# Kernel optimization log

Measured on AMD Instinct MI355X. Metric: run time of the kernel, lower is better.

## Reference

```python
import jax, jax.numpy as jnp
import numpy as np

L, B, E, H = 2048, 4, 1024, 8
D1 = 2 * E  # expand_ratio * embed_dim, already divisible by H
EPS = 1e-8


def setup_inputs() -> dict:
    key = jax.random.key(0)
    ks = jax.random.split(key, 12)
    std = 0.02
    return {
        "query": jax.random.normal(ks[0], (L, B, E), jnp.float32),
        "key": jax.random.normal(ks[1], (L, B, E), jnp.float32),
        "value": jax.random.normal(ks[2], (L, B, E), jnp.float32),
        "u_w": jax.random.normal(ks[3], (D1, E), jnp.float32) * std,
        "u_b": jax.random.normal(ks[4], (D1,), jnp.float32) * std,
        "v_w": jax.random.normal(ks[5], (D1, E), jnp.float32) * std,
        "v_b": jax.random.normal(ks[6], (D1,), jnp.float32) * std,
        "o_w": jax.random.normal(ks[7], (E, D1), jnp.float32) * std,
        "o_b": jax.random.normal(ks[8], (E,), jnp.float32) * std,
        # Toeplitz relative-position coefficients: t_0 (zero), t_1..t_{n-1} (pos), t_{-1}..t_{-(n-1)} (neg)
        "pos": jax.random.normal(ks[9], (H, L - 1), jnp.float32) * std,
        "zero": jax.random.normal(ks[10], (H, 1), jnp.float32) * std,
        "neg": jax.random.normal(ks[11], (H, L - 1), jnp.float32) * std,
    }


def _toeplitz_mix(v, pos, zero, neg):
    # v: (b, h, n, d). y_i = sum_j t_{i-j} v_j via circular conv of length 2n.
    b, h, n, d = v.shape
    m = 2 * n
    # a[0]=t_0, a[1:n]=t_1..t_{n-1}, a[n]=0 (unused), a[n+1:2n]=t_{-(n-1)}..t_{-1}
    a = jnp.concatenate([zero, pos[:, : n - 1], jnp.zeros((h, 1), v.dtype), neg[:, : n - 1][:, ::-1]], axis=-1)
    af = jnp.fft.rfft(a, n=m, axis=-1)            # (h, n+1)
    vf = jnp.fft.rfft(v, n=m, axis=-2)            # (b, h, n+1, d)
    y = jnp.fft.irfft(af[None, :, :, None] * vf, n=m, axis=-2)
    return y[:, :, :n, :]


def reference(query, key, value, u_w, u_b, v_w, v_b, o_w, o_b, pos, zero, neg):
    n, b, e = query.shape
    # SimpleRMSNorm: x / (||x||_2 / sqrt(d) + eps)
    rms = jnp.linalg.norm(query, axis=-1, keepdims=True) * (e ** -0.5)
    x = query / (rms + EPS)
    u = jax.nn.silu(jnp.einsum("nbe,fe->nbf", x, u_w) + u_b)   # (n, b, d1)
    v = jax.nn.silu(jnp.einsum("nbe,fe->nbf", x, v_w) + v_b)   # (n, b, d1)
    hd = v.shape[-1] // H
    vh = v.reshape(n, b, H, hd).transpose(1, 2, 0, 3)          # (b, h, n, d)
    y = _toeplitz_mix(vh, pos, zero, neg)                      # (b, h, n, d)
    y = y.transpose(2, 0, 1, 3).reshape(n, b, H * hd)          # (n, b, d1)
    out = u * y
    return jnp.einsum("nbf,ef->nbe", out, o_w) + o_b + query
```

## Files before the change

kernel.cpp:

```cpp
#include <hip/hip_runtime.h>
#include <math.h>

typedef unsigned short u16;
typedef __bf16 bf16x8 __attribute__((ext_vector_type(8)));
typedef float f32x4 __attribute__((ext_vector_type(4)));

#define LSEQ 2048
#define NB   4
#define NE   1024
#define NHEAD 8
#define ND1  2048
#define NHD  256
#define NM   8192
#define CRP  4104

__device__ __forceinline__ u16 f2bf(float f) {
  unsigned u = __float_as_uint(f);
  u += 0x7FFFu + ((u >> 16) & 1u);
  return (u16)(u >> 16);
}
__device__ __forceinline__ float bf2f(u16 h) {
  return __uint_as_float(((unsigned)h) << 16);
}

__device__ __forceinline__ void gl_lds16(const u16* g, u16* l) {
  __builtin_amdgcn_global_load_lds(
      (const __attribute__((address_space(1))) void*)g,
      (__attribute__((address_space(3))) void*)l, 16, 0, 0);
}

__global__ __launch_bounds__(256) void cvt_kernel(const float* __restrict__ src,
                                                  u16* __restrict__ dst, int n4) {
  int i = blockIdx.x * 256 + threadIdx.x;
  if (i < n4) {
    float4 v = ((const float4*)src)[i];
    ushort4 o;
    o.x = f2bf(v.x); o.y = f2bf(v.y); o.z = f2bf(v.z); o.w = f2bf(v.w);
    ((ushort4*)dst)[i] = o;
  }
}

__global__ __launch_bounds__(256) void build_cr8(const float* __restrict__ pos,
                                                 const float* __restrict__ zero,
                                                 const float* __restrict__ neg,
                                                 u16* __restrict__ cr8) {
  int h = blockIdx.x >> 3, s = blockIdx.x & 7;
  u16* out = cr8 + (size_t)blockIdx.x * CRP;
  for (int m = threadIdx.x; m < CRP; m += 256) {
    int mm = m + s;
    float val = 0.f;
    if (mm <= 4094) {
      int t = 2047 - mm;
      if (t == 0)      val = zero[h];
      else if (t > 0)  val = pos[h * (LSEQ - 1) + t - 1];
      else             val = neg[h * (LSEQ - 1) + (-t) - 1];
    }
    out[m] = f2bf(val);
  }
}

__global__ __launch_bounds__(256) void rmsnorm_kernel(const float* __restrict__ q,
                                                      u16* __restrict__ x) {
  int row = blockIdx.x;
  float4 v = ((const float4*)(q + (size_t)row * NE))[threadIdx.x];
  float ss = v.x * v.x + v.y * v.y + v.z * v.z + v.w * v.w;
  #pragma unroll
  for (int off = 32; off > 0; off >>= 1) ss += __shfl_down(ss, off, 64);
  __shared__ float wss[4];
  int wave = threadIdx.x >> 6, lane = threadIdx.x & 63;
  if (lane == 0) wss[wave] = ss;
  __syncthreads();
  float tot = wss[0] + wss[1] + wss[2] + wss[3];
  float scale = 1.f / (sqrtf(tot) * 0.03125f + 1e-8f);
  ushort4 o;
  o.x = f2bf(v.x * scale); o.y = f2bf(v.y * scale);
  o.z = f2bf(v.z * scale); o.w = f2bf(v.w * scale);
  ((ushort4*)(x + (size_t)row * NE))[threadIdx.x] = o;
}

__global__ __launch_bounds__(256) void transpose_v(const u16* __restrict__ v,
                                                   u16* __restrict__ vT) {
  __shared__ u16 s[64 * 66];
  int j0 = blockIdx.x * 64, d0 = blockIdx.y * 64;
  int h = blockIdx.z >> 2, b = blockIdx.z & 3;
  #pragma unroll
  for (int it = 0; it < 16; ++it) {
    int idx = threadIdx.x + 256 * it;
    int r = idx >> 6, c = idx & 63;
    s[r * 66 + c] = v[((size_t)(j0 + r) * NB + b) * ND1 + h * NHD + d0 + c];
  }
  __syncthreads();
  #pragma unroll
  for (int it = 0; it < 16; ++it) {
    int idx = threadIdx.x + 256 * it;
    int r = idx >> 6, c = idx & 63;
    vT[((size_t)h * (NB * NHD) + b * NHD + d0 + r) * LSEQ + j0 + c] = s[c * 66 + r];
  }
}


__device__ __forceinline__ bf16x8 ldsfrag(const u16* buf, int rr, int q) {
  return *(const bf16x8*)(buf + rr * 64 + ((q ^ (rr & 7)) * 8));
}

template <int MODE>
__device__ __forceinline__ void stage_Ah(const u16* A, const u16* Acr, int Ksz,
                                         int i0, int kt, int half, u16* dstbuf,
                                         int tid) {
  int wave = tid >> 6;
  #pragma unroll
  for (int it = 0; it < 2; ++it) {
    int vv = it * 512 + tid;
    int r = vv >> 3, c8 = vv & 7, c8s = c8 ^ (r & 7);
    int row = i0 + half * 128 + r;
    const u16* src;
    if (MODE != 1) {
      src = A + (size_t)row * Ksz + kt * 64 + c8s * 8;
    } else {
      int p = 2047 - row + kt * 64;
      int s = p & 7, qq = p - s;
      src = Acr + (size_t)s * CRP + qq + c8s * 8;
    }
    gl_lds16(src, dstbuf + half * 8192 + (it * 512 + wave * 64) * 8);
  }
}

__device__ __forceinline__ void stage_Bh(const u16* B, int Ksz, int n0, int kt,
                                         int half, u16* dstbuf, int tid) {
  int wave = tid >> 6;
  #pragma unroll
  for (int it = 0; it < 2; ++it) {
    int vv = it * 512 + tid;
    int r = vv >> 3, c8 = vv & 7, c8s = c8 ^ (r & 7);
    gl_lds16(B + (size_t)(n0 + half * 128 + r) * Ksz + kt * 64 + c8s * 8,
             dstbuf + half * 8192 + (it * 512 + wave * 64) * 8);
  }
}

#define PHASE_MID()                                        \
  __builtin_amdgcn_s_barrier();                            \
  asm volatile("s_waitcnt lgkmcnt(0)" ::: "memory");       \
  __builtin_amdgcn_sched_barrier(0);                       \
  __builtin_amdgcn_s_setprio(1);

#define PHASE_END()                                        \
  __builtin_amdgcn_s_setprio(0);                           \
  __builtin_amdgcn_s_barrier();                            \
  __builtin_amdgcn_sched_barrier(0);

template <int MODE>
__global__ __launch_bounds__(512, 2) void gemm256(
    const u16* __restrict__ A, const u16* __restrict__ Bw,
    const float* __restrict__ bias, u16* __restrict__ Cbf,
    int Msz, int Nsz, int Ksz) {
  extern __shared__ __align__(16) u16 lds[];
  u16* As = lds;
  u16* Ws = lds + 32768;

  const int tid = threadIdx.x;
  const int lane = tid & 63, wave = tid >> 6;
  const int wr = (wave >> 2) * 128, wc = (wave & 3) * 64;
  const int lr = lane & 15, lq = lane >> 4;
  const int i0 = blockIdx.y * 256, n0 = blockIdx.x * 256;

  const u16* Bh = Bw;
  const u16* Acr = A;
  if (MODE == 1) {
    Bh  = Bw + (size_t)blockIdx.z * Nsz * Ksz;
    Acr = A + (size_t)blockIdx.z * 8 * CRP;
  }
  const int nkt = Ksz >> 6;

  f32x4 acc[8][4];
  #pragma unroll
  for (int a = 0; a < 8; ++a)
    #pragma unroll
    for (int b = 0; b < 4; ++b) acc[a][b] = (f32x4){0.f, 0.f, 0.f, 0.f};

  stage_Ah<MODE>(A, Acr, Ksz, i0, 0, 0, As, tid);
  stage_Ah<MODE>(A, Acr, Ksz, i0, 0, 1, As, tid);
  stage_Bh(Bh, Ksz, n0, 0, 0, Ws, tid);
  stage_Bh(Bh, Ksz, n0, 0, 1, Ws, tid);
  stage_Bh(Bh, Ksz, n0, 1, 0, Ws + 16384, tid);
  stage_Bh(Bh, Ksz, n0, 1, 1, Ws + 16384, tid);
  asm volatile("s_waitcnt vmcnt(4)" ::: "memory");
  __builtin_amdgcn_s_barrier();
  __builtin_amdgcn_sched_barrier(0);

  for (int tt = 0; tt < nkt; ++tt) {
    const int cur = tt & 1;
    const u16* Ab = As + cur * 16384;
    const u16* Wb = Ws + cur * 16384;
    u16* An = As + (cur ^ 1) * 16384;
    u16* Wn = Ws + cur * 16384;

    bf16x8 a[4][2], b[2][2], b2[2][2];

    #pragma unroll
    for (int rt = 0; rt < 4; ++rt) {
      int ar = wr + rt * 16 + lr;
      a[rt][0] = ldsfrag(Ab, ar, lq);
      a[rt][1] = ldsfrag(Ab, ar, 4 + lq);
    }
    #pragma unroll
    for (int ct = 0; ct < 2; ++ct) {
      int br = wc + ct * 16 + lr;
      b[ct][0] = ldsfrag(Wb, br, lq);
      b[ct][1] = ldsfrag(Wb, br, 4 + lq);
    }
    if (tt + 1 < nkt) stage_Ah<MODE>(A, Acr, Ksz, i0, tt + 1, 0, An, tid);
    PHASE_MID();
    #pragma unroll
    for (int rt = 0; rt < 4; ++rt)
      #pragma unroll
      for (int ct = 0; ct < 2; ++ct) {
        acc[rt][ct] = __builtin_amdgcn_mfma_f32_16x16x32_bf16(a[rt][0], b[ct][0], acc[rt][ct], 0, 0, 0);
        acc[rt][ct] = __builtin_amdgcn_mfma_f32_16x16x32_bf16(a[rt][1], b[ct][1], acc[rt][ct], 0, 0, 0);
      }
    PHASE_END();

    #pragma unroll
    for (int ct = 0; ct < 2; ++ct) {
      int br = wc + (ct + 2) * 16 + lr;
      b2[ct][0] = ldsfrag(Wb, br, lq);
      b2[ct][1] = ldsfrag(Wb, br, 4 + lq);
    }
    if (tt + 1 < nkt) stage_Ah<MODE>(A, Acr, Ksz, i0, tt + 1, 1, An, tid);
    PHASE_MID();
    #pragma unroll
    for (int rt = 0; rt < 4; ++rt)
      #pragma unroll
      for (int ct = 0; ct < 2; ++ct) {
        acc[rt][ct + 2] = __builtin_amdgcn_mfma_f32_16x16x32_bf16(a[rt][0], b2[ct][0], acc[rt][ct + 2], 0, 0, 0);
        acc[rt][ct + 2] = __builtin_amdgcn_mfma_f32_16x16x32_bf16(a[rt][1], b2[ct][1], acc[rt][ct + 2], 0, 0, 0);
      }
    PHASE_END();

    #pragma unroll
    for (int rt = 0; rt < 4; ++rt) {
      int ar = wr + (rt + 4) * 16 + lr;
      a[rt][0] = ldsfrag(Ab, ar, lq);
      a[rt][1] = ldsfrag(Ab, ar, 4 + lq);
    }
    if (tt + 2 < nkt) stage_Bh(Bh, Ksz, n0, tt + 2, 0, Wn, tid);
    PHASE_MID();
    #pragma unroll
    for (int rt = 0; rt < 4; ++rt)
      #pragma unroll
      for (int ct = 0; ct < 2; ++ct) {
        acc[rt + 4][ct + 2] = __builtin_amdgcn_mfma_f32_16x16x32_bf16(a[rt][0], b2[ct][0], acc[rt + 4][ct + 2], 0, 0, 0);
        acc[rt + 4][ct + 2] = __builtin_amdgcn_mfma_f32_16x16x32_bf16(a[rt][1], b2[ct][1], acc[rt + 4][ct + 2], 0, 0, 0);
      }
    PHASE_END();

    if (tt + 2 < nkt) stage_Bh(Bh, Ksz, n0, tt + 2, 1, Wn, tid);
    if (tt == nkt - 2) { asm volatile("s_waitcnt vmcnt(0)" ::: "memory"); }
    else               { asm volatile("s_waitcnt vmcnt(4)" ::: "memory"); }
    PHASE_MID();
    #pragma unroll
    for (int rt = 0; rt < 4; ++rt)
      #pragma unroll
      for (int ct = 0; ct < 2; ++ct) {
        acc[rt + 4][ct] = __builtin_amdgcn_mfma_f32_16x16x32_bf16(a[rt][0], b[ct][0], acc[rt + 4][ct], 0, 0, 0);
        acc[rt + 4][ct] = __builtin_amdgcn_mfma_f32_16x16x32_bf16(a[rt][1], b[ct][1], acc[rt + 4][ct], 0, 0, 0);
      }
    PHASE_END();
  }

  #pragma unroll
  for (int rt = 0; rt < 8; ++rt) {
    #pragma unroll
    for (int ct = 0; ct < 4; ++ct) {
      int col = n0 + wc + ct * 16 + lr;
      #pragma unroll
      for (int reg = 0; reg < 4; ++reg) {
        int row = i0 + wr + rt * 16 + lq * 4 + reg;
        float yv = acc[rt][ct][reg];
        if (MODE == 0) {
          float t = yv + bias[col];
          t = t / (1.f + __expf(-t));
          Cbf[(size_t)row * Nsz + col] = f2bf(t);
        } else {
          int b = col >> 8, d = col & 255;
          size_t ui = ((size_t)row * NB + b) * ND1 + (size_t)blockIdx.z * NHD + d;
          float uv = bf2f(Cbf[ui]);
          Cbf[ui] = f2bf(uv * yv);
        }
      }
    }
  }
}

template <int MODE>
__global__ __launch_bounds__(256) void gemm_kernel(
    const u16* __restrict__ A, const u16* __restrict__ Bw,
    const float* __restrict__ bias, const float* __restrict__ resid,
    u16* __restrict__ Cbf, float* __restrict__ Cf,
    int Msz, int Nsz, int Ksz) {
  __shared__ __align__(16) u16 As[128 * 64];
  __shared__ __align__(16) u16 Ws[128 * 64];

  const int tid = threadIdx.x;
  const int lane = tid & 63, wave = tid >> 6;
  const int wr = (wave >> 1) * 64, wc = (wave & 1) * 64;
  const int lr = lane & 15, lq = lane >> 4;
  const int i0 = blockIdx.y * 128, n0 = blockIdx.x * 128;

  f32x4 acc[4][4];
  #pragma unroll
  for (int a = 0; a < 4; ++a)
    #pragma unroll
    for (int b = 0; b < 4; ++b) acc[a][b] = (f32x4){0.f, 0.f, 0.f, 0.f};

  const int nkt = Ksz >> 6;
  for (int kt = 0; kt < nkt; ++kt) {
    #pragma unroll
    for (int it = 0; it < 4; ++it) {
      int vv = tid + 256 * it;
      int r = vv >> 3, c8 = vv & 7;
      int c8s = c8 ^ (r & 7);
      gl_lds16(A + (size_t)(i0 + r) * Ksz + kt * 64 + c8s * 8,
               &As[(size_t)(wave * 64 + it * 256) * 8]);
    }
    #pragma unroll
    for (int it = 0; it < 4; ++it) {
      int vv = tid + 256 * it;
      int r = vv >> 3, c8 = vv & 7;
      int c8s = c8 ^ (r & 7);
      gl_lds16(Bw + (size_t)(n0 + r) * Ksz + kt * 64 + c8s * 8,
               &Ws[(size_t)(wave * 64 + it * 256) * 8]);
    }
    __syncthreads();
    #pragma unroll
    for (int ks = 0; ks < 2; ++ks) {
      bf16x8 af[4], bfr[4];
      #pragma unroll
      for (int rt = 0; rt < 4; ++rt) {
        int ar = wr + rt * 16 + lr;
        int cq = (ks * 4 + lq) ^ (ar & 7);
        af[rt] = *(const bf16x8*)&As[ar * 64 + cq * 8];
      }
      #pragma unroll
      for (int ct = 0; ct < 4; ++ct) {
        int br = wc + ct * 16 + lr;
        int cq = (ks * 4 + lq) ^ (br & 7);
        bfr[ct] = *(const bf16x8*)&Ws[br * 64 + cq * 8];
      }
      #pragma unroll
      for (int rt = 0; rt < 4; ++rt)
        #pragma unroll
        for (int ct = 0; ct < 4; ++ct)
          acc[rt][ct] = __builtin_amdgcn_mfma_f32_16x16x32_bf16(
              af[rt], bfr[ct], acc[rt][ct], 0, 0, 0);
    }
    __syncthreads();
  }

  #pragma unroll
  for (int rt = 0; rt < 4; ++rt) {
    #pragma unroll
    for (int ct = 0; ct < 4; ++ct) {
      int col = n0 + wc + ct * 16 + lr;
      #pragma unroll
      for (int reg = 0; reg < 4; ++reg) {
        int row = i0 + wr + rt * 16 + lq * 4 + reg;
        float yv = acc[rt][ct][reg];
        size_t oi = (size_t)row * Nsz + col;
        Cf[oi] = yv + bias[col] + resid[oi];
      }
    }
  }
}

extern "C" void kernel_launch(void* const* d_in, const int* in_sizes, int n_in,
                              void* d_out, int out_size, void* d_ws, size_t ws_size,
                              hipStream_t stream) {
  const float* q    = (const float*)d_in[0];
  const float* uw   = (const float*)d_in[3];
  const float* ub   = (const float*)d_in[4];
  const float* vw   = (const float*)d_in[5];
  const float* vb   = (const float*)d_in[6];
  const float* ow   = (const float*)d_in[7];
  const float* ob   = (const float*)d_in[8];
  const float* pos  = (const float*)d_in[9];
  const float* zero = (const float*)d_in[10];
  const float* neg  = (const float*)d_in[11];
  float* out = (float*)d_out;

  char* ws = (char*)d_ws;
  u16* x   = (u16*)(ws + 0);
  u16* uwb = (u16*)(ws + 16777216);
  u16* vwb = (u16*)(ws + 20971520);
  u16* owb = (u16*)(ws + 25165824);
  u16* u   = (u16*)(ws + 29360128);
  u16* v   = (u16*)(ws + 62914560);
  u16* vT  = (u16*)(ws + 96468992);
  u16* cr8 = (u16*)(ws + 130023424);

  hipFuncSetAttribute((const void*)gemm256<0>,
                      hipFuncAttributeMaxDynamicSharedMemorySize, 131072);
  hipFuncSetAttribute((const void*)gemm256<1>,
                      hipFuncAttributeMaxDynamicSharedMemorySize, 131072);

  cvt_kernel<<<2048, 256, 0, stream>>>(uw, uwb, 524288);
  cvt_kernel<<<2048, 256, 0, stream>>>(vw, vwb, 524288);
  cvt_kernel<<<2048, 256, 0, stream>>>(ow, owb, 524288);
  build_cr8<<<64, 256, 0, stream>>>(pos, zero, neg, cr8);
  rmsnorm_kernel<<<NM, 256, 0, stream>>>(q, x);

  gemm256<0><<<dim3(8, 32, 1), 512, 131072, stream>>>(x, uwb, ub, u, NM, ND1, NE);
  gemm256<0><<<dim3(8, 32, 1), 512, 131072, stream>>>(x, vwb, vb, v, NM, ND1, NE);
  transpose_v<<<dim3(32, 4, 32), 256, 0, stream>>>(v, vT);
  gemm256<1><<<dim3(4, 8, 8), 512, 131072, stream>>>(cr8, vT, nullptr, u,
                                                     LSEQ, NB * NHD, LSEQ);
  gemm_kernel<2><<<dim3(8, 64, 1), 256, 0, stream>>>(u, owb, ob, q, nullptr, out,
                                                     NM, NE, ND1);
}
```

Before: 373.2 us.

## Merge prep kernels, batch U/V GEMMs, restage epilogue through LDS, vectorize transpose

Merges the three weight conversions and the Toeplitz-coefficient build into one launch, and runs the U and V projections as a single grid with a z-dimension that picks the weight, bias and output. The 256-tile GEMM main loop drops from four phases to two per k-step, loading all B fragments at once. The epilogue goes through a swizzled LDS tile so global stores and the u*y multiply use 16-byte vector accesses. The transpose now uses ushort4 loads and stores. Together these aim to cut launch count and scattered 2-byte stores, at the cost of more registers and less interleaving of loads with MFMA work.

```diff
diff --git a/kernel.cpp b/kernel.cpp
--- a/kernel.cpp
+++ b/kernel.cpp
@@ -22,6 +22,11 @@
 __device__ __forceinline__ float bf2f(u16 h) {
   return __uint_as_float(((unsigned)h) << 16);
 }
+__device__ __forceinline__ unsigned mulbf2(unsigned y2, unsigned u2) {
+  float ylo = bf2f((u16)(y2 & 0xFFFF)), yhi = bf2f((u16)(y2 >> 16));
+  float ulo = bf2f((u16)(u2 & 0xFFFF)), uhi = bf2f((u16)(u2 >> 16));
+  return (unsigned)f2bf(ylo * ulo) | ((unsigned)f2bf(yhi * uhi) << 16);
+}
 
 __device__ __forceinline__ void gl_lds16(const u16* g, u16* l) {
   __builtin_amdgcn_global_load_lds(
@@ -29,33 +34,36 @@
       (__attribute__((address_space(3))) void*)l, 16, 0, 0);
 }
 
-__global__ __launch_bounds__(256) void cvt_kernel(const float* __restrict__ src,
-                                                  u16* __restrict__ dst, int n4) {
-  int i = blockIdx.x * 256 + threadIdx.x;
-  if (i < n4) {
-    float4 v = ((const float4*)src)[i];
+__global__ __launch_bounds__(256) void prep_kernel(
+    const float* __restrict__ uw, const float* __restrict__ vw,
+    const float* __restrict__ ow, u16* __restrict__ uwb, u16* __restrict__ vwb,
+    u16* __restrict__ owb, const float* __restrict__ pos,
+    const float* __restrict__ zero, const float* __restrict__ neg,
+    u16* __restrict__ cr8) {
+  int bx = blockIdx.x;
+  if (bx < 6144) {
+    const float* s = bx < 2048 ? uw : (bx < 4096 ? vw : ow);
+    u16* d = bx < 2048 ? uwb : (bx < 4096 ? vwb : owb);
+    int i = (bx & 2047) * 256 + threadIdx.x;
+    float4 v = ((const float4*)s)[i];
     ushort4 o;
     o.x = f2bf(v.x); o.y = f2bf(v.y); o.z = f2bf(v.z); o.w = f2bf(v.w);
-    ((ushort4*)dst)[i] = o;
-  }
-}
-
-__global__ __launch_bounds__(256) void build_cr8(const float* __restrict__ pos,
-                                                 const float* __restrict__ zero,
-                                                 const float* __restrict__ neg,
-                                                 u16* __restrict__ cr8) {
-  int h = blockIdx.x >> 3, s = blockIdx.x & 7;
-  u16* out = cr8 + (size_t)blockIdx.x * CRP;
-  for (int m = threadIdx.x; m < CRP; m += 256) {
-    int mm = m + s;
-    float val = 0.f;
-    if (mm <= 4094) {
-      int t = 2047 - mm;
-      if (t == 0)      val = zero[h];
-      else if (t > 0)  val = pos[h * (LSEQ - 1) + t - 1];
-      else             val = neg[h * (LSEQ - 1) + (-t) - 1];
-    }
-    out[m] = f2bf(val);
+    ((ushort4*)d)[i] = o;
+  } else {
+    int bb = bx - 6144;
+    int h = bb >> 3, sh = bb & 7;
+    u16* out = cr8 + (size_t)bb * CRP;
+    for (int m = threadIdx.x; m < CRP; m += 256) {
+      int mm = m + sh;
+      float val = 0.f;
+      if (mm <= 4094) {
+        int t = 2047 - mm;
+        if (t == 0)      val = zero[h];
+        else if (t > 0)  val = pos[h * (LSEQ - 1) + t - 1];
+        else             val = neg[h * (LSEQ - 1) + (-t) - 1];
+      }
+      out[m] = f2bf(val);
+    }
   }
 }
 
@@ -80,21 +88,27 @@
 
 __global__ __launch_bounds__(256) void transpose_v(const u16* __restrict__ v,
                                                    u16* __restrict__ vT) {
-  __shared__ u16 s[64 * 66];
+  __shared__ u16 s[64 * 68];
   int j0 = blockIdx.x * 64, d0 = blockIdx.y * 64;
   int h = blockIdx.z >> 2, b = blockIdx.z & 3;
   #pragma unroll
-  for (int it = 0; it < 16; ++it) {
-    int idx = threadIdx.x + 256 * it;
-    int r = idx >> 6, c = idx & 63;
-    s[r * 66 + c] = v[((size_t)(j0 + r) * NB + b) * ND1 + h * NHD + d0 + c];
+  for (int it = 0; it < 4; ++it) {
+    int idx = it * 256 + threadIdx.x;
+    int r = idx >> 4, c4 = idx & 15;
+    *(ushort4*)&s[r * 68 + c4 * 4] =
+        *(const ushort4*)&v[((size_t)(j0 + r) * NB + b) * ND1 + h * NHD + d0 + c4 * 4];
   }
   __syncthreads();
   #pragma unroll
-  for (int it = 0; it < 16; ++it) {
-    int idx = threadIdx.x + 256 * it;
-    int r = idx >> 6, c = idx & 63;
-    vT[((size_t)h * (NB * NHD) + b * NHD + d0 + r) * LSEQ + j0 + c] = s[c * 66 + r];
+  for (int it = 0; it < 4; ++it) {
+    int idx = it * 256 + threadIdx.x;
+    int cc = idx >> 4, jq = idx & 15;
+    ushort4 o;
+    o.x = s[(jq * 4 + 0) * 68 + cc];
+    o.y = s[(jq * 4 + 1) * 68 + cc];
+    o.z = s[(jq * 4 + 2) * 68 + cc];
+    o.w = s[(jq * 4 + 3) * 68 + cc];
+    *(ushort4*)&vT[((size_t)h * (NB * NHD) + b * NHD + d0 + cc) * LSEQ + j0 + jq * 4] = o;
   }
 }
 
@@ -150,9 +164,10 @@
 
 template <int MODE>
 __global__ __launch_bounds__(512, 2) void gemm256(
-    const u16* __restrict__ A, const u16* __restrict__ Bw,
-    const float* __restrict__ bias, u16* __restrict__ Cbf,
-    int Msz, int Nsz, int Ksz) {
+    const u16* __restrict__ A, const u16* __restrict__ Bw0,
+    const u16* __restrict__ Bw1, const float* __restrict__ bias0,
+    const float* __restrict__ bias1, u16* __restrict__ C0,
+    u16* __restrict__ C1, int Msz, int Nsz, int Ksz) {
   extern __shared__ __align__(16) u16 lds[];
   u16* As = lds;
   u16* Ws = lds + 32768;
@@ -163,10 +178,16 @@
   const int lr = lane & 15, lq = lane >> 4;
   const int i0 = blockIdx.y * 256, n0 = blockIdx.x * 256;
 
-  const u16* Bh = Bw;
+  const u16* Bh;
   const u16* Acr = A;
-  if (MODE == 1) {
-    Bh  = Bw + (size_t)blockIdx.z * Nsz * Ksz;
+  const float* bias = bias0;
+  u16* Cp = C0;
+  if (MODE == 0) {
+    Bh = blockIdx.z ? Bw1 : Bw0;
+    bias = blockIdx.z ? bias1 : bias0;
+    Cp = blockIdx.z ? C1 : C0;
+  } else {
+    Bh  = Bw0 + (size_t)blockIdx.z * Nsz * Ksz;
     Acr = A + (size_t)blockIdx.z * 8 * CRP;
   }
   const int nkt = Ksz >> 6;
@@ -194,7 +215,7 @@
     u16* An = As + (cur ^ 1) * 16384;
     u16* Wn = Ws + cur * 16384;
 
-    bf16x8 a[4][2], b[2][2], b2[2][2];
+    bf16x8 a[4][2], b[4][2];
 
     #pragma unroll
     for (int rt = 0; rt < 4; ++rt) {
@@ -203,36 +224,22 @@
       a[rt][1] = ldsfrag(Ab, ar, 4 + lq);
     }
     #pragma unroll
-    for (int ct = 0; ct < 2; ++ct) {
+    for (int ct = 0; ct < 4; ++ct) {
       int br = wc + ct * 16 + lr;
       b[ct][0] = ldsfrag(Wb, br, lq);
       b[ct][1] = ldsfrag(Wb, br, 4 + lq);
     }
-    if (tt + 1 < nkt) stage_Ah<MODE>(A, Acr, Ksz, i0, tt + 1, 0, An, tid);
+    if (tt + 1 < nkt) {
+      stage_Ah<MODE>(A, Acr, Ksz, i0, tt + 1, 0, An, tid);
+      stage_Ah<MODE>(A, Acr, Ksz, i0, tt + 1, 1, An, tid);
+    }
     PHASE_MID();
     #pragma unroll
     for (int rt = 0; rt < 4; ++rt)
       #pragma unroll
-      for (int ct = 0; ct < 2; ++ct) {
+      for (int ct = 0; ct < 4; ++ct) {
         acc[rt][ct] = __builtin_amdgcn_mfma_f32_16x16x32_bf16(a[rt][0], b[ct][0], acc[rt][ct], 0, 0, 0);
         acc[rt][ct] = __builtin_amdgcn_mfma_f32_16x16x32_bf16(a[rt][1], b[ct][1], acc[rt][ct], 0, 0, 0);
-      }
-    PHASE_END();
-
-    #pragma unroll
-    for (int ct = 0; ct < 2; ++ct) {
-      int br = wc + (ct + 2) * 16 + lr;
-      b2[ct][0] = ldsfrag(Wb, br, lq);
-      b2[ct][1] = ldsfrag(Wb, br, 4 + lq);
-    }
-    if (tt + 1 < nkt) stage_Ah<MODE>(A, Acr, Ksz, i0, tt + 1, 1, An, tid);
-    PHASE_MID();
-    #pragma unroll
-    for (int rt = 0; rt < 4; ++rt)
-      #pragma unroll
-      for (int ct = 0; ct < 2; ++ct) {
-        acc[rt][ct + 2] = __builtin_amdgcn_mfma_f32_16x16x32_bf16(a[rt][0], b2[ct][0], acc[rt][ct + 2], 0, 0, 0);
-        acc[rt][ct + 2] = __builtin_amdgcn_mfma_f32_16x16x32_bf16(a[rt][1], b2[ct][1], acc[rt][ct + 2], 0, 0, 0);
       }
     PHASE_END();
 
@@ -242,61 +249,68 @@
       a[rt][0] = ldsfrag(Ab, ar, lq);
       a[rt][1] = ldsfrag(Ab, ar, 4 + lq);
     }
-    if (tt + 2 < nkt) stage_Bh(Bh, Ksz, n0, tt + 2, 0, Wn, tid);
-    PHASE_MID();
-    #pragma unroll
-    for (int rt = 0; rt < 4; ++rt)
-      #pragma unroll
-      for (int ct = 0; ct < 2; ++ct) {
-        acc[rt + 4][ct + 2] = __builtin_amdgcn_mfma_f32_16x16x32_bf16(a[rt][0], b2[ct][0], acc[rt + 4][ct + 2], 0, 0, 0);
-        acc[rt + 4][ct + 2] = __builtin_amdgcn_mfma_f32_16x16x32_bf16(a[rt][1], b2[ct][1], acc[rt + 4][ct + 2], 0, 0, 0);
-      }
-    PHASE_END();
-
-    if (tt + 2 < nkt) stage_Bh(Bh, Ksz, n0, tt + 2, 1, Wn, tid);
+    if (tt + 2 < nkt) {
+      stage_Bh(Bh, Ksz, n0, tt + 2, 0, Wn, tid);
+      stage_Bh(Bh, Ksz, n0, tt + 2, 1, Wn, tid);
+    }
     if (tt == nkt - 2) { asm volatile("s_waitcnt vmcnt(0)" ::: "memory"); }
     else               { asm volatile("s_waitcnt vmcnt(4)" ::: "memory"); }
     PHASE_MID();
     #pragma unroll
     for (int rt = 0; rt < 4; ++rt)
       #pragma unroll
-      for (int ct = 0; ct < 2; ++ct) {
+      for (int ct = 0; ct < 4; ++ct) {
         acc[rt + 4][ct] = __builtin_amdgcn_mfma_f32_16x16x32_bf16(a[rt][0], b[ct][0], acc[rt + 4][ct], 0, 0, 0);
         acc[rt + 4][ct] = __builtin_amdgcn_mfma_f32_16x16x32_bf16(a[rt][1], b[ct][1], acc[rt + 4][ct], 0, 0, 0);
       }
     PHASE_END();
   }
 
+  __syncthreads();
+  u16* zl = lds;
   #pragma unroll
   for (int rt = 0; rt < 8; ++rt) {
     #pragma unroll
     for (int ct = 0; ct < 4; ++ct) {
-      int col = n0 + wc + ct * 16 + lr;
+      int col_l = wc + ct * 16 + lr;
       #pragma unroll
       for (int reg = 0; reg < 4; ++reg) {
-        int row = i0 + wr + rt * 16 + lq * 4 + reg;
+        int row_l = wr + rt * 16 + lq * 4 + reg;
         float yv = acc[rt][ct][reg];
         if (MODE == 0) {
-          float t = yv + bias[col];
-          t = t / (1.f + __expf(-t));
-          Cbf[(size_t)row * Nsz + col] = f2bf(t);
-        } else {
-          int b = col >> 8, d = col & 255;
-          size_t ui = ((size_t)row * NB + b) * ND1 + (size_t)blockIdx.z * NHD + d;
-          float uv = bf2f(Cbf[ui]);
-          Cbf[ui] = f2bf(uv * yv);
+          float t = yv + bias[n0 + col_l];
+          yv = t / (1.f + __expf(-t));
         }
-      }
-    }
-  }
-}
-
-template <int MODE>
-__global__ __launch_bounds__(256) void gemm_kernel(
+        zl[row_l * 256 + (col_l ^ (((row_l >> 2) & 3) << 4))] = f2bf(yv);
+      }
+    }
+  }
+  __syncthreads();
+  #pragma unroll
+  for (int k = 0; k < 16; ++k) {
+    int cc = k * 512 + tid;
+    int row_l = cc >> 5, c8 = cc & 31;
+    int colbase = c8 * 8;
+    int swz = colbase ^ (((row_l >> 2) & 3) << 4);
+    uint4 y4 = *(uint4*)&zl[row_l * 256 + swz];
+    if (MODE == 0) {
+      *(uint4*)&Cp[(size_t)(i0 + row_l) * Nsz + n0 + colbase] = y4;
+    } else {
+      size_t ui = ((size_t)(i0 + row_l) * NB + blockIdx.x) * ND1 +
+                  (size_t)blockIdx.z * NHD + colbase;
+      uint4 u4 = *(const uint4*)&Cp[ui];
+      uint4 o;
+      o.x = mulbf2(y4.x, u4.x); o.y = mulbf2(y4.y, u4.y);
+      o.z = mulbf2(y4.z, u4.z); o.w = mulbf2(y4.w, u4.w);
+      *(uint4*)&Cp[ui] = o;
+    }
+  }
+}
+
+__global__ __launch_bounds__(256) void gemm_out(
     const u16* __restrict__ A, const u16* __restrict__ Bw,
     const float* __restrict__ bias, const float* __restrict__ resid,
-    u16* __restrict__ Cbf, float* __restrict__ Cf,
-    int Msz, int Nsz, int Ksz) {
+    float* __restrict__ Cf, int Nsz, int Ksz) {
   __shared__ __align__(16) u16 As[128 * 64];
   __shared__ __align__(16) u16 Ws[128 * 64];
 
@@ -364,9 +378,8 @@
       #pragma unroll
       for (int reg = 0; reg < 4; ++reg) {
         int row = i0 + wr + rt * 16 + lq * 4 + reg;
-        float yv = acc[rt][ct][reg];
         size_t oi = (size_t)row * Nsz + col;
-        Cf[oi] = yv + bias[col] + resid[oi];
+        Cf[oi] = acc[rt][ct][reg] + bias[col] + resid[oi];
       }
     }
   }
@@ -402,17 +415,15 @@
   hipFuncSetAttribute((const void*)gemm256<1>,
                       hipFuncAttributeMaxDynamicSharedMemorySize, 131072);
 
-  cvt_kernel<<<2048, 256, 0, stream>>>(uw, uwb, 524288);
-  cvt_kernel<<<2048, 256, 0, stream>>>(vw, vwb, 524288);
-  cvt_kernel<<<2048, 256, 0, stream>>>(ow, owb, 524288);
-  build_cr8<<<64, 256, 0, stream>>>(pos, zero, neg, cr8);
+  prep_kernel<<<6208, 256, 0, stream>>>(uw, vw, ow, uwb, vwb, owb,
+                                        pos, zero, neg, cr8);
   rmsnorm_kernel<<<NM, 256, 0, stream>>>(q, x);
 
-  gemm256<0><<<dim3(8, 32, 1), 512, 131072, stream>>>(x, uwb, ub, u, NM, ND1, NE);
-  gemm256<0><<<dim3(8, 32, 1), 512, 131072, stream>>>(x, vwb, vb, v, NM, ND1, NE);
+  gemm256<0><<<dim3(8, 32, 2), 512, 131072, stream>>>(x, uwb, vwb, ub, vb, u, v,
+                                                      NM, ND1, NE);
   transpose_v<<<dim3(32, 4, 32), 256, 0, stream>>>(v, vT);
-  gemm256<1><<<dim3(4, 8, 8), 512, 131072, stream>>>(cr8, vT, nullptr, u,
+  gemm256<1><<<dim3(4, 8, 8), 512, 131072, stream>>>(cr8, vT, nullptr, nullptr,
+                                                     nullptr, u, nullptr,
                                                      LSEQ, NB * NHD, LSEQ);
-  gemm_kernel<2><<<dim3(8, 64, 1), 256, 0, stream>>>(u, owb, ob, q, nullptr, out,
-                                                     NM, NE, ND1);
-}
+  gemm_out<<<dim3(8, 64, 1), 256, 0, stream>>>(u, owb, ob, q, out, NE, ND1);
+}
```

Result: no change. 368.5 us (-1.2%).
